# Kernel optimization log

Hardware: AMD Instinct MI355X
Metric: run time of the kernel (lower is better)

## Reference

```python
import jax, jax.numpy as jnp
import numpy as np

B, T, U, E, P, C = 32, 4096, 1024, 512, 512, 4
LN_EPS = 1e-5


def setup_inputs() -> dict:
    key = jax.random.key(0)
    k = jax.random.split(key, 6)
    enc_out = jax.random.normal(k[0], (B, T, E), dtype=jnp.float32)
    pred_out = jax.random.normal(k[1], (B, U, P), dtype=jnp.float32)
    frame_label = jax.random.randint(k[2], (B, T), 0, C)
    frame_tlabel = jax.random.randint(k[3], (B, U), 0, C)
    # every emotion id appears in each sample's label list (dense [B, C])
    label = jnp.tile(jnp.arange(C), (B, 1))
    # LayerNorm params (torch defaults: weight=1, bias=0)
    norm_w = jnp.ones((E + P,), dtype=jnp.float32)
    norm_b = jnp.zeros((E + P,), dtype=jnp.float32)
    # Linear head params
    head_w = jax.random.normal(k[4], (C, E + P), dtype=jnp.float32) * 0.02
    head_b = jnp.zeros((C,), dtype=jnp.float32)
    return {
        "enc_out": enc_out, "pred_out": pred_out,
        "frame_label": frame_label, "frame_tlabel": frame_tlabel,
        "label": label,
        "norm_w": norm_w, "norm_b": norm_b,
        "head_w": head_w, "head_b": head_b,
    }


def _masked_mean(x, ids, n_cls):
    # x: [B, S, D]; ids: [B, S] -> per-class mean [B, C, D] via one-hot segment-sum
    onehot = (ids[:, :, None] == jnp.arange(n_cls)[None, None, :]).astype(x.dtype)  # [B,S,C]
    cnt = onehot.sum(axis=1)                                   # [B, C]
    summed = jnp.einsum('bsc,bsd->bcd', onehot, x)             # [B, C, D]
    return summed / jnp.maximum(cnt, 1.0)[..., None]


def reference(enc_out, pred_out, frame_label, frame_tlabel, label, norm_w, norm_b, head_w, head_b):
    n_cls = head_w.shape[0]
    enc_mean = _masked_mean(enc_out, frame_label, n_cls)    # [B, C, E]
    pred_mean = _masked_mean(pred_out, frame_tlabel, n_cls)  # [B, C, P]
    feat = jnp.concatenate([enc_mean, pred_mean], axis=-1)   # [B, C, E+P]
    # LayerNorm over last dim
    mu = feat.mean(axis=-1, keepdims=True)
    var = jnp.mean((feat - mu) ** 2, axis=-1, keepdims=True)
    feat_n = (feat - mu) / jnp.sqrt(var + LN_EPS) * norm_w + norm_b
    logits = jnp.einsum('bcd,nd->bcn', feat_n, head_w) + head_b  # [B, C, n_cls]
    logp = jax.nn.log_softmax(logits, axis=-1)
    # loss += -log_softmax(head(norm(cat)))[emo] for each emo in label[i]
    bb, ll = label.shape
    sel = logp[jnp.arange(bb)[:, None], label, label]  # [B, L]
    loss = -sel.sum() / (bb * ll)
    return loss
```

## Files before the change

kernel.cpp:

```cpp
#include <hip/hip_runtime.h>
#include <math.h>

#define C_CLS 4
#define D_HALF 512
#define D4 128
#define DFEAT 1024
#define BB 32

__global__ void count_kernel(const int* __restrict__ fl, const int* __restrict__ ftl,
                             int T, int U, float* __restrict__ cnt) {
    int b = blockIdx.x;
    int which = blockIdx.y;
    const int* lab = (which == 0) ? (fl + (size_t)b * T) : (ftl + (size_t)b * U);
    int n = (which == 0) ? T : U;
    __shared__ int h[C_CLS];
    if (threadIdx.x < C_CLS) h[threadIdx.x] = 0;
    __syncthreads();
    int h0 = 0, h1 = 0, h2 = 0, h3 = 0;
    for (int i = threadIdx.x; i < n; i += blockDim.x) {
        int c = lab[i];
        h0 += (c == 0); h1 += (c == 1); h2 += (c == 2); h3 += (c == 3);
    }
    if (h0) atomicAdd(&h[0], h0);
    if (h1) atomicAdd(&h[1], h1);
    if (h2) atomicAdd(&h[2], h2);
    if (h3) atomicAdd(&h[3], h3);
    __syncthreads();
    if (threadIdx.x < C_CLS)
        cnt[((size_t)which * gridDim.x + b) * C_CLS + threadIdx.x] = (float)h[threadIdx.x];
}

__global__ void masked_sum_fused(const float* __restrict__ enc, const float* __restrict__ pred,
                                 const int* __restrict__ fl, const int* __restrict__ ftl,
                                 float* __restrict__ enc_part, float* __restrict__ pred_part,
                                 int T, int U, int SE, int SP) {
    int bid = blockIdx.x;
    const float* x; const int* labels; float* partial;
    int Tlen, splits, b, s;
    if (bid < BB * SE) {
        x = enc; labels = fl; partial = enc_part; Tlen = T; splits = SE;
        b = bid / SE; s = bid % SE;
    } else {
        int idx = bid - BB * SE;
        x = pred; labels = ftl; partial = pred_part; Tlen = U; splits = SP;
        b = idx / SP; s = idx % SP;
    }
    int len = Tlen / splits;
    int t0 = s * len;
    int tx = threadIdx.x & 127;
    int ty = threadIdx.x >> 7;

    __shared__ int lab[256];
    const int* labg = labels + (size_t)b * Tlen + t0;
    for (int i = threadIdx.x; i < len; i += 256) lab[i] = labg[i];
    __syncthreads();

    const float4* x4 = (const float4*)x + ((size_t)b * Tlen + t0) * D4 + tx;
    float4 acc[C_CLS];
#pragma unroll
    for (int k = 0; k < C_CLS; k++) acc[k] = make_float4(0.f, 0.f, 0.f, 0.f);

    for (int t = ty; t < len; t += 2) {
        float4 v = x4[(size_t)t * D4];
        int c = lab[t];
#pragma unroll
        for (int k = 0; k < C_CLS; k++) {
            float m = (c == k) ? 1.0f : 0.0f;
            acc[k].x = fmaf(v.x, m, acc[k].x);
            acc[k].y = fmaf(v.y, m, acc[k].y);
            acc[k].z = fmaf(v.z, m, acc[k].z);
            acc[k].w = fmaf(v.w, m, acc[k].w);
        }
    }

    __shared__ float4 cbuf[C_CLS][D4];
    if (ty == 1) {
#pragma unroll
        for (int k = 0; k < C_CLS; k++) cbuf[k][tx] = acc[k];
    }
    __syncthreads();
    if (ty == 0) {
        float4* out = (float4*)partial + (size_t)(b * splits + s) * C_CLS * D4 + tx;
#pragma unroll
        for (int k = 0; k < C_CLS; k++) {
            float4 o = acc[k], p = cbuf[k][tx];
            o.x += p.x; o.y += p.y; o.z += p.z; o.w += p.w;
            out[(size_t)k * D4] = o;
        }
    }
}

__device__ __forceinline__ float blockReduceSum256(float v) {
    __shared__ float red[4];
#pragma unroll
    for (int off = 32; off > 0; off >>= 1) v += __shfl_down(v, off);
    int wid = threadIdx.x >> 6, lane = threadIdx.x & 63;
    __syncthreads();
    if (lane == 0) red[wid] = v;
    __syncthreads();
    return red[0] + red[1] + red[2] + red[3];
}

__global__ void finalize_kernel(const float* __restrict__ enc_part,
                                const float* __restrict__ pred_part,
                                const float* __restrict__ cnt,
                                const float* __restrict__ norm_w, const float* __restrict__ norm_b,
                                const float* __restrict__ head_w, const float* __restrict__ head_b,
                                float* __restrict__ diag, int B, int SE, int SP) {
    int b = blockIdx.x;
    int c = blockIdx.y;
    __shared__ float feat[DFEAT];
    float cnt_e = fmaxf(cnt[((size_t)0 * B + b) * C_CLS + c], 1.0f);
    float cnt_p = fmaxf(cnt[((size_t)1 * B + b) * C_CLS + c], 1.0f);

    for (int d = threadIdx.x; d < D_HALF; d += 256) {
        float s = 0.f;
        for (int sp = 0; sp < SE; sp++)
            s += enc_part[((size_t)(b * SE + sp) * C_CLS + c) * D_HALF + d];
        feat[d] = s / cnt_e;
    }
    for (int d = threadIdx.x; d < D_HALF; d += 256) {
        float s = 0.f;
        for (int sp = 0; sp < SP; sp++)
            s += pred_part[((size_t)(b * SP + sp) * C_CLS + c) * D_HALF + d];
        feat[D_HALF + d] = s / cnt_p;
    }
    __syncthreads();

    float lsum = 0.f;
    for (int d = threadIdx.x; d < DFEAT; d += 256) lsum += feat[d];
    float mu = blockReduceSum256(lsum) * (1.0f / DFEAT);

    float lvar = 0.f;
    for (int d = threadIdx.x; d < DFEAT; d += 256) {
        float t = feat[d] - mu;
        lvar = fmaf(t, t, lvar);
    }
    float var = blockReduceSum256(lvar) * (1.0f / DFEAT);
    float rstd = rsqrtf(var + 1e-5f);

    float part[C_CLS] = {0.f, 0.f, 0.f, 0.f};
    for (int d = threadIdx.x; d < DFEAT; d += 256) {
        float fn = (feat[d] - mu) * rstd * norm_w[d] + norm_b[d];
#pragma unroll
        for (int n = 0; n < C_CLS; n++)
            part[n] = fmaf(fn, head_w[(size_t)n * DFEAT + d], part[n]);
    }
    float logits[C_CLS];
#pragma unroll
    for (int n = 0; n < C_CLS; n++)
        logits[n] = blockReduceSum256(part[n]) + head_b[n];

    if (threadIdx.x == 0) {
        float m = fmaxf(fmaxf(logits[0], logits[1]), fmaxf(logits[2], logits[3]));
        float se = 0.f;
#pragma unroll
        for (int n = 0; n < C_CLS; n++) se += expf(logits[n] - m);
        float lse = m + logf(se);
        diag[b * C_CLS + c] = logits[c] - lse;
    }
}

__global__ void loss_kernel(const float* __restrict__ diag, const int* __restrict__ label,
                            float* __restrict__ out, int B) {
    int i = threadIdx.x;
    float v = 0.f;
    if (i < B * C_CLS) {
        int b = i / C_CLS;
        int j = label[i];
        v = diag[b * C_CLS + j];
    }
#pragma unroll
    for (int off = 32; off > 0; off >>= 1) v += __shfl_down(v, off);
    __shared__ float red[2];
    int wid = i >> 6, lane = i & 63;
    if (lane == 0) red[wid] = v;
    __syncthreads();
    if (i == 0) out[0] = -(red[0] + red[1]) / (float)(B * C_CLS);
}

extern "C" void kernel_launch(void* const* d_in, const int* in_sizes, int n_in,
                              void* d_out, int out_size, void* d_ws, size_t ws_size,
                              hipStream_t stream) {
    const float* enc_out      = (const float*)d_in[0];
    const float* pred_out     = (const float*)d_in[1];
    const int*   frame_label  = (const int*)d_in[2];
    const int*   frame_tlabel = (const int*)d_in[3];
    const int*   label        = (const int*)d_in[4];
    const float* norm_w       = (const float*)d_in[5];
    const float* norm_b       = (const float*)d_in[6];
    const float* head_w       = (const float*)d_in[7];
    const float* head_b       = (const float*)d_in[8];
    float* out = (float*)d_out;

    const int B = BB, T = 4096, U = 1024;
    int SE = 64, SP = 32;
    auto need = [&](int se, int sp) -> size_t {
        return ((size_t)B * se * C_CLS * D_HALF + (size_t)B * sp * C_CLS * D_HALF
                + 2 * B * C_CLS + B * C_CLS) * sizeof(float);
    };
    while (need(SE, SP) > ws_size && SE > 16) { SE >>= 1; if (SP > 4) SP >>= 1; }

    float* ws        = (float*)d_ws;
    float* enc_part  = ws;
    float* pred_part = enc_part + (size_t)B * SE * C_CLS * D_HALF;
    float* cnt       = pred_part + (size_t)B * SP * C_CLS * D_HALF;
    float* diag      = cnt + 2 * B * C_CLS;

    count_kernel<<<dim3(B, 2), 256, 0, stream>>>(frame_label, frame_tlabel, T, U, cnt);
    masked_sum_fused<<<B * SE + B * SP, 256, 0, stream>>>(enc_out, pred_out,
                                                          frame_label, frame_tlabel,
                                                          enc_part, pred_part, T, U, SE, SP);
    finalize_kernel<<<dim3(B, C_CLS), 256, 0, stream>>>(enc_part, pred_part, cnt,
                                                        norm_w, norm_b, head_w, head_b,
                                                        diag, B, SE, SP);
    loss_kernel<<<1, 128, 0, stream>>>(diag, label, out, B);
}
```

Before: 479.1 us.

## Fuse count and loss kernels into finalize, unroll masked-sum with nontemporal loads

After: 436.8 us. -8.8%, faster.

```diff
diff --git a/kernel.cpp b/kernel.cpp
--- a/kernel.cpp
+++ b/kernel.cpp
@@ -7,34 +7,16 @@
 #define DFEAT 1024
 #define BB 32
 
-__global__ void count_kernel(const int* __restrict__ fl, const int* __restrict__ ftl,
-                             int T, int U, float* __restrict__ cnt) {
-    int b = blockIdx.x;
-    int which = blockIdx.y;
-    const int* lab = (which == 0) ? (fl + (size_t)b * T) : (ftl + (size_t)b * U);
-    int n = (which == 0) ? T : U;
-    __shared__ int h[C_CLS];
-    if (threadIdx.x < C_CLS) h[threadIdx.x] = 0;
-    __syncthreads();
-    int h0 = 0, h1 = 0, h2 = 0, h3 = 0;
-    for (int i = threadIdx.x; i < n; i += blockDim.x) {
-        int c = lab[i];
-        h0 += (c == 0); h1 += (c == 1); h2 += (c == 2); h3 += (c == 3);
-    }
-    if (h0) atomicAdd(&h[0], h0);
-    if (h1) atomicAdd(&h[1], h1);
-    if (h2) atomicAdd(&h[2], h2);
-    if (h3) atomicAdd(&h[3], h3);
-    __syncthreads();
-    if (threadIdx.x < C_CLS)
-        cnt[((size_t)which * gridDim.x + b) * C_CLS + threadIdx.x] = (float)h[threadIdx.x];
-}
+typedef float f4 __attribute__((ext_vector_type(4)));
 
 __global__ void masked_sum_fused(const float* __restrict__ enc, const float* __restrict__ pred,
                                  const int* __restrict__ fl, const int* __restrict__ ftl,
                                  float* __restrict__ enc_part, float* __restrict__ pred_part,
+                                 float* __restrict__ out,
                                  int T, int U, int SE, int SP) {
     int bid = blockIdx.x;
+    if (bid == 0 && threadIdx.x == 0) out[0] = 0.0f;
+
     const float* x; const int* labels; float* partial;
     int Tlen, splits, b, s;
     if (bid < BB * SE) {
@@ -55,38 +37,40 @@
     for (int i = threadIdx.x; i < len; i += 256) lab[i] = labg[i];
     __syncthreads();
 
-    const float4* x4 = (const float4*)x + ((size_t)b * Tlen + t0) * D4 + tx;
-    float4 acc[C_CLS];
+    const f4* x4 = (const f4*)x + ((size_t)b * Tlen + t0) * D4 + tx;
+    f4 acc[C_CLS];
 #pragma unroll
-    for (int k = 0; k < C_CLS; k++) acc[k] = make_float4(0.f, 0.f, 0.f, 0.f);
+    for (int k = 0; k < C_CLS; k++) acc[k] = (f4){0.f, 0.f, 0.f, 0.f};
 
-    for (int t = ty; t < len; t += 2) {
-        float4 v = x4[(size_t)t * D4];
+    int t = ty;
+    for (; t + 2 < len; t += 4) {
+        f4 v0 = __builtin_nontemporal_load(&x4[(size_t)t * D4]);
+        f4 v1 = __builtin_nontemporal_load(&x4[(size_t)(t + 2) * D4]);
+        int c0 = lab[t], c1 = lab[t + 2];
+#pragma unroll
+        for (int k = 0; k < C_CLS; k++) {
+            acc[k] += v0 * (float)(c0 == k);
+            acc[k] += v1 * (float)(c1 == k);
+        }
+    }
+    for (; t < len; t += 2) {
+        f4 v = __builtin_nontemporal_load(&x4[(size_t)t * D4]);
         int c = lab[t];
 #pragma unroll
-        for (int k = 0; k < C_CLS; k++) {
-            float m = (c == k) ? 1.0f : 0.0f;
-            acc[k].x = fmaf(v.x, m, acc[k].x);
-            acc[k].y = fmaf(v.y, m, acc[k].y);
-            acc[k].z = fmaf(v.z, m, acc[k].z);
-            acc[k].w = fmaf(v.w, m, acc[k].w);
-        }
+        for (int k = 0; k < C_CLS; k++) acc[k] += v * (float)(c == k);
     }
 
-    __shared__ float4 cbuf[C_CLS][D4];
+    __shared__ f4 cbuf[C_CLS][D4];
     if (ty == 1) {
 #pragma unroll
         for (int k = 0; k < C_CLS; k++) cbuf[k][tx] = acc[k];
     }
     __syncthreads();
     if (ty == 0) {
-        float4* out = (float4*)partial + (size_t)(b * splits + s) * C_CLS * D4 + tx;
+        f4* o4 = (f4*)partial + (size_t)(b * splits + s) * C_CLS * D4 + tx;
 #pragma unroll
-        for (int k = 0; k < C_CLS; k++) {
-            float4 o = acc[k], p = cbuf[k][tx];
-            o.x += p.x; o.y += p.y; o.z += p.z; o.w += p.w;
-            out[(size_t)k * D4] = o;
-        }
+        for (int k = 0; k < C_CLS; k++)
+            o4[(size_t)k * D4] = acc[k] + cbuf[k][tx];
     }
 }
 
@@ -101,18 +85,28 @@
     return red[0] + red[1] + red[2] + red[3];
 }
 
-__global__ void finalize_kernel(const float* __restrict__ enc_part,
-                                const float* __restrict__ pred_part,
-                                const float* __restrict__ cnt,
-                                const float* __restrict__ norm_w, const float* __restrict__ norm_b,
-                                const float* __restrict__ head_w, const float* __restrict__ head_b,
-                                float* __restrict__ diag, int B, int SE, int SP) {
+__global__ void finalize_loss_kernel(const float* __restrict__ enc_part,
+                                     const float* __restrict__ pred_part,
+                                     const int* __restrict__ fl, const int* __restrict__ ftl,
+                                     const int* __restrict__ label,
+                                     const float* __restrict__ norm_w, const float* __restrict__ norm_b,
+                                     const float* __restrict__ head_w, const float* __restrict__ head_b,
+                                     float* __restrict__ out,
+                                     int T, int U, int B, int SE, int SP) {
     int b = blockIdx.x;
     int c = blockIdx.y;
+
+    int ce = 0, cp = 0;
+    {
+        const int* p = fl + (size_t)b * T;
+        for (int i = threadIdx.x; i < T; i += 256) ce += (p[i] == c);
+        const int* q = ftl + (size_t)b * U;
+        for (int i = threadIdx.x; i < U; i += 256) cp += (q[i] == c);
+    }
+    float cnt_e = fmaxf(blockReduceSum256((float)ce), 1.0f);
+    float cnt_p = fmaxf(blockReduceSum256((float)cp), 1.0f);
+
     __shared__ float feat[DFEAT];
-    float cnt_e = fmaxf(cnt[((size_t)0 * B + b) * C_CLS + c], 1.0f);
-    float cnt_p = fmaxf(cnt[((size_t)1 * B + b) * C_CLS + c], 1.0f);
-
     for (int d = threadIdx.x; d < D_HALF; d += 256) {
         float s = 0.f;
         for (int sp = 0; sp < SE; sp++)
@@ -156,27 +150,13 @@
         float se = 0.f;
 #pragma unroll
         for (int n = 0; n < C_CLS; n++) se += expf(logits[n] - m);
-        float lse = m + logf(se);
-        diag[b * C_CLS + c] = logits[c] - lse;
+        float lp = logits[c] - (m + logf(se));
+        int occ = 0;
+#pragma unroll
+        for (int l = 0; l < C_CLS; l++) occ += (label[b * C_CLS + l] == c);
+        if (occ)
+            atomicAdd(out, -lp * (float)occ * (1.0f / (BB * C_CLS)));
     }
-}
-
-__global__ void loss_kernel(const float* __restrict__ diag, const int* __restrict__ label,
-                            float* __restrict__ out, int B) {
-    int i = threadIdx.x;
-    float v = 0.f;
-    if (i < B * C_CLS) {
-        int b = i / C_CLS;
-        int j = label[i];
-        v = diag[b * C_CLS + j];
-    }
-#pragma unroll
-    for (int off = 32; off > 0; off >>= 1) v += __shfl_down(v, off);
-    __shared__ float red[2];
-    int wid = i >> 6, lane = i & 63;
-    if (lane == 0) red[wid] = v;
-    __syncthreads();
-    if (i == 0) out[0] = -(red[0] + red[1]) / (float)(B * C_CLS);
 }
 
 extern "C" void kernel_launch(void* const* d_in, const int* in_sizes, int n_in,
@@ -196,23 +176,20 @@
     const int B = BB, T = 4096, U = 1024;
     int SE = 64, SP = 32;
     auto need = [&](int se, int sp) -> size_t {
-        return ((size_t)B * se * C_CLS * D_HALF + (size_t)B * sp * C_CLS * D_HALF
-                + 2 * B * C_CLS + B * C_CLS) * sizeof(float);
+        return ((size_t)B * se * C_CLS * D_HALF + (size_t)B * sp * C_CLS * D_HALF)
+               * sizeof(float);
     };
     while (need(SE, SP) > ws_size && SE > 16) { SE >>= 1; if (SP > 4) SP >>= 1; }
 
-    float* ws        = (float*)d_ws;
-    float* enc_part  = ws;
+    float* enc_part  = (float*)d_ws;
     float* pred_part = enc_part + (size_t)B * SE * C_CLS * D_HALF;
-    float* cnt       = pred_part + (size_t)B * SP * C_CLS * D_HALF;
-    float* diag      = cnt + 2 * B * C_CLS;
 
-    count_kernel<<<dim3(B, 2), 256, 0, stream>>>(frame_label, frame_tlabel, T, U, cnt);
     masked_sum_fused<<<B * SE + B * SP, 256, 0, stream>>>(enc_out, pred_out,
                                                           frame_label, frame_tlabel,
-                                                          enc_part, pred_part, T, U, SE, SP);
-    finalize_kernel<<<dim3(B, C_CLS), 256, 0, stream>>>(enc_part, pred_part, cnt,
-                                                        norm_w, norm_b, head_w, head_b,
-                                                        diag, B, SE, SP);
-    loss_kernel<<<1, 128, 0, stream>>>(diag, label, out, B);
+                                                          enc_part, pred_part, out,
+                                                          T, U, SE, SP);
+    finalize_loss_kernel<<<dim3(B, C_CLS), 256, 0, stream>>>(enc_part, pred_part,
+                                                             frame_label, frame_tlabel, label,
+                                                             norm_w, norm_b, head_w, head_b,
+                                                             out, T, U, B, SE, SP);
 }
```
